# Optimization experiments

Measured on AMD Instinct MI355X. Metric: run time of the kernel, lower is better.

## Reference

```python
import jax, jax.numpy as jnp
import numpy as np

B, LAGS, POOL, D, H, NTS = 16, 4096, 4, 512, 8, 1000
S = LAGS // POOL          # num_pools = 1024
DH = D // H               # head dim = 64


def _layernorm_dim1(x, gamma, beta, eps=1e-5):
    # torch code: mean/var over dim=1 (channel axis), unbiased var, per-position affine
    mean = jnp.mean(x, axis=1, keepdims=True)
    var = jnp.var(x, axis=1, keepdims=True, ddof=1)
    unit = (x - mean) / jnp.sqrt(eps + var)
    return gamma * unit + beta


def setup_inputs() -> dict:
    key = jax.random.key(0)
    ks = jax.random.split(key, 16)
    inp = {
        "ts": jax.random.normal(ks[0], (B, 1, LAGS), dtype=jnp.float32),
        "te": jax.random.randint(ks[1], (B, 1), 0, NTS),
        "conv_w": jax.random.normal(ks[2], (D, 1, POOL), dtype=jnp.float32) * (1.0 / POOL) ** 0.5,
        "conv_b": jax.random.normal(ks[3], (D,), dtype=jnp.float32) * 0.02,
        "pe_emb": jax.random.normal(ks[4], (S, D), dtype=jnp.float32),
        "ts_emb": jax.random.normal(ks[5], (NTS, D), dtype=jnp.float32),
        "ln1_g": jnp.ones((S,), dtype=jnp.float32),
        "ln1_b": jnp.zeros((S,), dtype=jnp.float32),
        "dense_M": jax.random.normal(ks[6], (D, D), dtype=jnp.float32) * D ** -0.5,
        "Wq": jax.random.normal(ks[7], (H, DH, D), dtype=jnp.float32) * D ** -0.5,
        "Wk": jax.random.normal(ks[8], (H, DH, D), dtype=jnp.float32) * D ** -0.5,
        "Wv": jax.random.normal(ks[9], (H, DH, D), dtype=jnp.float32) * D ** -0.5,
        "Wo": jax.random.normal(ks[10], (D, D), dtype=jnp.float32) * D ** -0.5,
        "bo": jnp.zeros((D, 1), dtype=jnp.float32),
        "ln2_g": jnp.ones((S,), dtype=jnp.float32),
        "ln2_b": jnp.zeros((S,), dtype=jnp.float32),
    }
    return inp


def _forward(ts, te, conv_w, conv_b, pe_emb, ts_emb, ln1_g, ln1_b,
             dense_M, Wq, Wk, Wv, Wo, bo, ln2_g, ln2_b):
    # Conv1d with stride == kernel_size: non-overlapping patches
    xr = ts.reshape(B, S, POOL)                                   # (B,S,P)
    conv = jnp.einsum('bsp,dp->bds', xr, conv_w[:, 0, :]) + conv_b[:, None]  # (B,D,S)
    conv = conv + pe_emb.T                                        # positional add (D,S)
    act = jax.nn.gelu(conv, approximate=False)
    n1 = _layernorm_dim1(act, ln1_g, ln1_b)
    dense = jnp.einsum('ed,bds->bes', dense_M, n1)                # Linear: M @ x
    dense = dense + ts_emb[te[:, 0]][:, :, None]                  # ts embedding (B,D,1)

    # multi-head attention, Q=K=V=dense; vectorized over heads
    Qd = jnp.einsum('hcd,bds->bhcs', Wq, dense)                   # (B,H,DH,S)
    Kd = jnp.einsum('hcd,bds->bhcs', Wk, dense)
    Vd = jnp.einsum('hcd,bds->bhcs', Wv, dense)
    scores = jnp.einsum('bhci,bhcj->bhij', Qd, Kd) / DH ** 0.5    # (B,H,S,S)
    i_idx = jnp.arange(S)
    mask = i_idx[:, None] > i_idx[None, :]                        # tril(diagonal=-1): i>j -> -inf
    scores = jnp.where(mask, -jnp.inf, scores)
    sm = jax.nn.softmax(scores, axis=2)                           # softmax over dim 1 of (S,S)
    attn = jnp.einsum('bhci,bhij->bhcj', Vd, sm)                  # V @ softmaxed
    cat = attn.reshape(B, D, S)                                   # concat heads on dim 1
    out = jnp.einsum('ed,bds->bes', Wo, cat) + bo[None]           # final linear + bias
    res = out + conv                                              # residual
    return _layernorm_dim1(res, ln2_g, ln2_b)


def reference(ts, te, conv_w, conv_b, pe_emb, ts_emb, ln1_g, ln1_b,
              dense_M, Wq, Wk, Wv, Wo, bo, ln2_g, ln2_b):
    return _forward(ts, te, conv_w, conv_b, pe_emb, ts_emb, ln1_g, ln1_b,
                    dense_M, Wq, Wk, Wv, Wo, bo, ln2_g, ln2_b)
```

## Files before the change

kernel.cpp:

```cpp
#include <hip/hip_runtime.h>
#include <hip/hip_bf16.h>

#define B_ 16
#define S_ 1024
#define D_ 512
#define H_ 8
#define DH_ 64

typedef __attribute__((ext_vector_type(8))) short bf16x8;
typedef __attribute__((ext_vector_type(4))) short bf16x4;
typedef __attribute__((ext_vector_type(4))) float f32x4;
typedef __attribute__((ext_vector_type(16))) float f32x16;

__device__ __forceinline__ short f2bf(float f) {
    __hip_bfloat16 h = __float2bfloat16(f);
    return *reinterpret_cast<short*>(&h);
}
__device__ __forceinline__ unsigned pack_bf2(float lo, float hi) {
    unsigned a = (unsigned)(unsigned short)f2bf(lo);
    unsigned b = (unsigned)(unsigned short)f2bf(hi);
    return a | (b << 16);
}
__device__ __forceinline__ void gload16(const void* g, void* l) {
    __builtin_amdgcn_global_load_lds(
        (const __attribute__((address_space(1))) unsigned int*)g,
        (__attribute__((address_space(3))) unsigned int*)l, 16, 0, 0);
}

__global__ __launch_bounds__(256) void prep_w(
    const float* __restrict__ M, const float* __restrict__ Wq,
    const float* __restrict__ Wk, const float* __restrict__ Wv,
    const float* __restrict__ Wo, __hip_bfloat16* __restrict__ wb)
{
    const int gid = blockIdx.x * 256 + threadIdx.x;
    const int e8 = gid * 8;
    const int w = e8 >> 18;
    const int off = e8 & 262143;
    const float* src = (w == 0) ? M : (w == 1) ? Wq : (w == 2) ? Wk
                      : (w == 3) ? Wv : Wo;
    const float scale = (w == 1) ? 0.18033688011112042f : 1.0f;
    const float4 f0 = *reinterpret_cast<const float4*>(src + off);
    const float4 f1 = *reinterpret_cast<const float4*>(src + off + 4);
    union { short s[8]; bf16x8 v; } r;
    r.s[0] = f2bf(f0.x * scale); r.s[1] = f2bf(f0.y * scale);
    r.s[2] = f2bf(f0.z * scale); r.s[3] = f2bf(f0.w * scale);
    r.s[4] = f2bf(f1.x * scale); r.s[5] = f2bf(f1.y * scale);
    r.s[6] = f2bf(f1.z * scale); r.s[7] = f2bf(f1.w * scale);
    *reinterpret_cast<bf16x8*>(wb + e8) = r.v;
}

__global__ __launch_bounds__(256) void k1_conv_gelu_ln(
    const float* __restrict__ ts, const float* __restrict__ conv_w,
    const float* __restrict__ conv_b, const float* __restrict__ pe,
    const float* __restrict__ g1, const float* __restrict__ b1,
    __hip_bfloat16* __restrict__ n1)
{
    const int row = blockIdx.x;
    const int b = row >> 10, s = row & 1023;
    const int t = threadIdx.x;
    const float4 x = *reinterpret_cast<const float4*>(ts + b * 4096 + s * 4);

    float a[2];
#pragma unroll
    for (int k = 0; k < 2; ++k) {
        const int d = t + k * 256;
        const float4 w = *reinterpret_cast<const float4*>(conv_w + d * 4);
        float v = x.x * w.x + x.y * w.y + x.z * w.z + x.w * w.w
                + conv_b[d] + pe[s * 512 + d];
        a[k] = 0.5f * v * (1.0f + erff(v * 0.70710678118654752f));
    }
    float sum = a[0] + a[1], sq = a[0] * a[0] + a[1] * a[1];
#pragma unroll
    for (int off = 32; off > 0; off >>= 1) {
        sum += __shfl_down(sum, off);
        sq  += __shfl_down(sq, off);
    }
    __shared__ float rs[4], rq[4];
    const int wv = t >> 6, ln = t & 63;
    if (ln == 0) { rs[wv] = sum; rq[wv] = sq; }
    __syncthreads();
    sum = rs[0] + rs[1] + rs[2] + rs[3];
    sq  = rq[0] + rq[1] + rq[2] + rq[3];
    const float mean = sum * (1.0f / 512.0f);
    const float var  = (sq - 512.0f * mean * mean) * (1.0f / 511.0f);
    const float rstd = rsqrtf(var + 1e-5f);
    const float gg = g1[s], bb = b1[s];
#pragma unroll
    for (int k = 0; k < 2; ++k) {
        const int d = t + k * 256;
        n1[(size_t)row * 512 + d] = __float2bfloat16(gg * ((a[k] - mean) * rstd) + bb);
    }
}

template<int MODE>
__global__ __launch_bounds__(256) void gemm_k(
    const __hip_bfloat16* __restrict__ A,
    const __hip_bfloat16* __restrict__ Wb,
    void* __restrict__ outp,
    const float* __restrict__ aux,
    const int* __restrict__ te)
{
    __shared__ char lA[128 * 128];
    __shared__ char lB[128 * 128];

    const int t = threadIdx.x;
    const int lane = t & 63;
    const int w = t >> 6;
    const int wm = w & 1, wn = w >> 1;
    const int Rb = blockIdx.x * 128;
    const int Nb = blockIdx.y * 128;
    const int g = lane >> 4, lr = lane & 15;
    const int lrow = lane >> 3;
    const int coff = ((lane & 7) ^ lrow) * 8;

    f32x4 acc[4][4];
#pragma unroll
    for (int i = 0; i < 4; ++i)
#pragma unroll
        for (int j = 0; j < 4; ++j) acc[i][j] = {0.f, 0.f, 0.f, 0.f};

    for (int kt = 0; kt < 8; ++kt) {
        const int k0 = kt * 64;
#pragma unroll
        for (int i = 0; i < 4; ++i) {
            const int r0 = w * 32 + i * 8;
            gload16(A + (size_t)(Rb + r0 + lrow) * 512 + k0 + coff, lA + r0 * 128);
        }
#pragma unroll
        for (int i = 0; i < 4; ++i) {
            const int r0 = w * 32 + i * 8;
            gload16(Wb + (size_t)(Nb + r0 + lrow) * 512 + k0 + coff, lB + r0 * 128);
        }
        __syncthreads();
#pragma unroll
        for (int kk = 0; kk < 2; ++kk) {
            bf16x8 af[4], bfv[4];
            const int ch = kk * 4 + g;
#pragma unroll
            for (int mt = 0; mt < 4; ++mt) {
                const int row = wm * 64 + mt * 16 + lr;
                af[mt] = *reinterpret_cast<const bf16x8*>(
                    lA + row * 128 + ((ch ^ (row & 7)) << 4));
            }
#pragma unroll
            for (int nt = 0; nt < 4; ++nt) {
                const int row = wn * 64 + nt * 16 + lr;
                bfv[nt] = *reinterpret_cast<const bf16x8*>(
                    lB + row * 128 + ((ch ^ (row & 7)) << 4));
            }
#pragma unroll
            for (int mt = 0; mt < 4; ++mt)
#pragma unroll
                for (int nt = 0; nt < 4; ++nt)
                    acc[mt][nt] = __builtin_amdgcn_mfma_f32_16x16x32_bf16(
                        af[mt], bfv[nt], acc[mt][nt], 0, 0, 0);
        }
        __syncthreads();
    }

#pragma unroll
    for (int mt = 0; mt < 4; ++mt) {
#pragma unroll
        for (int nt = 0; nt < 4; ++nt) {
#pragma unroll
            for (int r = 0; r < 4; ++r) {
                const int R = Rb + wm * 64 + mt * 16 + 4 * g + r;
                const int N = Nb + wn * 64 + nt * 16 + lr;
                float v = acc[mt][nt][r];
                if (MODE == 0) {
                    const int b = R >> 10;
                    v += aux[(size_t)te[b] * 512 + N];
                    reinterpret_cast<__hip_bfloat16*>(outp)[(size_t)R * 512 + N] =
                        __float2bfloat16(v);
                } else if (MODE == 1) {
                    const int b = R >> 10, s = R & 1023, h = N >> 6, c = N & 63;
                    reinterpret_cast<__hip_bfloat16*>(outp)
                        [(((size_t)(b * 8 + h)) * 1024 + s) * 64 + c] = __float2bfloat16(v);
                } else if (MODE == 2) {
                    const int b = R >> 10, s = R & 1023, h = N >> 6, c = N & 63;
                    reinterpret_cast<__hip_bfloat16*>(outp)
                        [(((size_t)(b * 8 + h)) * 64 + c) * 1024 + s] = __float2bfloat16(v);
                } else {
                    reinterpret_cast<float*>(outp)[(size_t)R * 512 + N] = v + aux[N];
                }
            }
        }
    }
}

__device__ __forceinline__ void attn_step(
    const bf16x8 (&qf)[4], const bf16x8 (&kf)[4],
    const bf16x8& v00, const bf16x8& v01,
    const bf16x8& v10, const bf16x8& v11,
    const bool diag, const int l5, const int ln31,
    float& m, float& lsum, f32x16& o0, f32x16& o1)
{
    f32x16 sc;
#pragma unroll
    for (int r = 0; r < 16; ++r) sc[r] = 0.f;
#pragma unroll
    for (int kt = 0; kt < 4; ++kt)
        sc = __builtin_amdgcn_mfma_f32_32x32x16_bf16(qf[kt], kf[kt], sc, 0, 0, 0);

    float p[16];
    float mx = -3e38f;
    if (diag) {
#pragma unroll
        for (int r = 0; r < 16; ++r) {
            const int irow = (r & 3) + 8 * (r >> 2) + 4 * l5;
            const float v = (irow > ln31) ? -3e38f : sc[r];
            p[r] = v; mx = fmaxf(mx, v);
        }
    } else {
#pragma unroll
        for (int r = 0; r < 16; ++r) { p[r] = sc[r]; mx = fmaxf(mx, sc[r]); }
    }
    mx = fmaxf(mx, __shfl_xor(mx, 32));
    if (!__all(mx <= m + 8.0f)) {
        const float mn = fmaxf(m, mx);
        const float alpha = exp2f(m - mn);
        m = mn; lsum *= alpha;
#pragma unroll
        for (int r = 0; r < 16; ++r) {
            const int jrow = (r & 3) + 8 * (r >> 2) + 4 * l5;
            const float ar = __shfl(alpha, jrow);
            o0[r] *= ar; o1[r] *= ar;
        }
    }
    float ps = 0.f;
#pragma unroll
    for (int r = 0; r < 16; ++r) { p[r] = exp2f(p[r] - m); ps += p[r]; }
    ps += __shfl_xor(ps, 32);
    lsum += ps;

    union { unsigned u[4]; bf16x8 v; } pa0, pa1;
    pa0.u[0] = pack_bf2(p[0],  p[1]);  pa0.u[1] = pack_bf2(p[2],  p[3]);
    pa0.u[2] = pack_bf2(p[4],  p[5]);  pa0.u[3] = pack_bf2(p[6],  p[7]);
    pa1.u[0] = pack_bf2(p[8],  p[9]);  pa1.u[1] = pack_bf2(p[10], p[11]);
    pa1.u[2] = pack_bf2(p[12], p[13]); pa1.u[3] = pack_bf2(p[14], p[15]);
    o0 = __builtin_amdgcn_mfma_f32_32x32x16_bf16(pa0.v, v00, o0, 0, 0, 0);
    o0 = __builtin_amdgcn_mfma_f32_32x32x16_bf16(pa1.v, v01, o0, 0, 0, 0);
    o1 = __builtin_amdgcn_mfma_f32_32x32x16_bf16(pa0.v, v10, o1, 0, 0, 0);
    o1 = __builtin_amdgcn_mfma_f32_32x32x16_bf16(pa1.v, v11, o1, 0, 0, 0);
}

__device__ __forceinline__ void write_strip(
    __hip_bfloat16* __restrict__ dstbase, const int jw0,
    const f32x16& o0, const f32x16& o1, const float lsum,
    const int l5, const int ln31)
{
    const float linv = 1.0f / lsum;
#pragma unroll
    for (int r = 0; r < 16; ++r) {
        const int jrow = (r & 3) + 8 * (r >> 2) + 4 * l5;
        const float rinv = __shfl(linv, jrow);
        __hip_bfloat16* dst = dstbase + (size_t)(jw0 + jrow) * 512;
        dst[ln31]      = __float2bfloat16(o0[r] * rinv);
        dst[32 + ln31] = __float2bfloat16(o1[r] * rinv);
    }
}

__global__ __launch_bounds__(256, 2) void attn3_k(
    const __hip_bfloat16* __restrict__ Qm,
    const __hip_bfloat16* __restrict__ Km,
    const __hip_bfloat16* __restrict__ Vt,
    __hip_bfloat16* __restrict__ cat)
{
    const int t = threadIdx.x, lane = t & 63, w = t >> 6;
    const int l5 = lane >> 5, ln31 = lane & 31;
    const int bh = blockIdx.y;
    const int b = bh >> 3, h = bh & 7;
    const int sA = blockIdx.x * 4 + w;
    const int sB = 31 - sA;
    const int jA = sA * 32, jB = sB * 32;
    const int nA = sA + 1, nB = sB + 1;

    const __hip_bfloat16* Qh = Qm + (size_t)bh * (S_ * 64);
    const __hip_bfloat16* Kh = Km + (size_t)bh * (S_ * 64);
    const __hip_bfloat16* Vh = Vt + (size_t)bh * (64 * S_);

    bf16x8 kfA[4], kfB[4];
#pragma unroll
    for (int kt = 0; kt < 4; ++kt) {
        kfA[kt] = *reinterpret_cast<const bf16x8*>(
            Kh + (size_t)(jA + ln31) * 64 + kt * 16 + l5 * 8);
        kfB[kt] = *reinterpret_cast<const bf16x8*>(
            Kh + (size_t)(jB + ln31) * 64 + kt * 16 + l5 * 8);
    }

    f32x16 oA0, oA1, oB0, oB1;
#pragma unroll
    for (int r = 0; r < 16; ++r) { oA0[r] = 0.f; oA1[r] = 0.f; oB0[r] = 0.f; oB1[r] = 0.f; }
    float mA = -3e38f, lsA = 0.f, mB = -3e38f, lsB = 0.f;

    const __hip_bfloat16* Vr0 = Vh + (size_t)ln31 * S_;
    const __hip_bfloat16* Vr1 = Vh + (size_t)(32 + ln31) * S_;

    union u8 { bf16x4 h[2]; bf16x8 v; };
    bf16x8 qf[4]; u8 v00, v01, v10, v11;

    auto load_q = [&](int i0, bf16x8 (&dst)[4]) {
#pragma unroll
        for (int kt = 0; kt < 4; ++kt)
            dst[kt] = *reinterpret_cast<const bf16x8*>(
                Qh + (size_t)(i0 + ln31) * 64 + kt * 16 + l5 * 8);
    };
    auto load_v = [&](int i0, u8& a0, u8& a1, u8& a2, u8& a3) {
        const int b0 = i0 + 4 * l5, b1 = i0 + 16 + 4 * l5;
        a0.h[0] = *reinterpret_cast<const bf16x4*>(Vr0 + b0);
        a0.h[1] = *reinterpret_cast<const bf16x4*>(Vr0 + b0 + 8);
        a1.h[0] = *reinterpret_cast<const bf16x4*>(Vr0 + b1);
        a1.h[1] = *reinterpret_cast<const bf16x4*>(Vr0 + b1 + 8);
        a2.h[0] = *reinterpret_cast<const bf16x4*>(Vr1 + b0);
        a2.h[1] = *reinterpret_cast<const bf16x4*>(Vr1 + b0 + 8);
        a3.h[0] = *reinterpret_cast<const bf16x4*>(Vr1 + b1);
        a3.h[1] = *reinterpret_cast<const bf16x4*>(Vr1 + b1 + 8);
    };

    load_q(0, qf);
    load_v(0, v00, v01, v10, v11);

    for (int it = 0; it < nB; ++it) {
        const int ipf = (it + 1 < nB ? it + 1 : it) * 32;
        bf16x8 qn[4]; u8 n00, n01, n10, n11;
        load_q(ipf, qn);
        load_v(ipf, n00, n01, n10, n11);

        attn_step(qf, kfB, v00.v, v01.v, v10.v, v11.v,
                  it == nB - 1, l5, ln31, mB, lsB, oB0, oB1);
        if (it < nA)
            attn_step(qf, kfA, v00.v, v01.v, v10.v, v11.v,
                      it == nA - 1, l5, ln31, mA, lsA, oA0, oA1);

#pragma unroll
        for (int kt = 0; kt < 4; ++kt) qf[kt] = qn[kt];
        v00 = n00; v01 = n01; v10 = n10; v11 = n11;
    }

    __hip_bfloat16* dstbase = cat + (size_t)b * 1024 * 512 + h * 64;
    write_strip(dstbase, jA, oA0, oA1, lsA, l5, ln31);
    write_strip(dstbase, jB, oB0, oB1, lsB, l5, ln31);
}

__global__ __launch_bounds__(256) void k5_res_ln(
    const float* __restrict__ outf,
    const float* __restrict__ ts, const float* __restrict__ conv_w,
    const float* __restrict__ conv_b, const float* __restrict__ pe,
    const float* __restrict__ g2, const float* __restrict__ b2,
    float* __restrict__ out)
{
    __shared__ float tile[16 * 520];
    const int blk = blockIdx.x;
    const int b = blk >> 6, s0 = (blk & 63) * 16;
    const int t = threadIdx.x;
    const int sl = t >> 4, c = t & 15;
    const int s = s0 + sl;

    const float4 x = *reinterpret_cast<const float4*>(ts + b * 4096 + s * 4);
    float vals[32];
    float sum = 0.f, sq = 0.f;
#pragma unroll
    for (int j = 0; j < 32; ++j) {
        const int d = c + 16 * j;
        const float4 wv = *reinterpret_cast<const float4*>(conv_w + d * 4);
        const float conv = x.x * wv.x + x.y * wv.y + x.z * wv.z + x.w * wv.w
                         + conv_b[d] + pe[s * 512 + d];
        const float a = outf[(size_t)(b * 1024 + s) * 512 + d] + conv;
        vals[j] = a; sum += a; sq += a * a;
    }
#pragma unroll
    for (int off = 1; off < 16; off <<= 1) {
        sum += __shfl_xor(sum, off);
        sq  += __shfl_xor(sq, off);
    }
    const float mean = sum * (1.0f / 512.0f);
    const float var  = (sq - 512.0f * mean * mean) * (1.0f / 511.0f);
    const float rstd = rsqrtf(var + 1e-5f);
    const float gg = g2[s], bb = b2[s];
#pragma unroll
    for (int j = 0; j < 32; ++j) {
        const int d = c + 16 * j;
        tile[sl * 520 + d] = gg * ((vals[j] - mean) * rstd) + bb;
    }
    __syncthreads();
#pragma unroll
    for (int q2 = 0; q2 < 2; ++q2) {
        const int d = t + q2 * 256;
        float buf[16];
#pragma unroll
        for (int sl2 = 0; sl2 < 16; ++sl2) buf[sl2] = tile[sl2 * 520 + d];
        float4* dst = reinterpret_cast<float4*>(
            out + ((size_t)b * 512 + d) * 1024 + s0);
        dst[0] = make_float4(buf[0],  buf[1],  buf[2],  buf[3]);
        dst[1] = make_float4(buf[4],  buf[5],  buf[6],  buf[7]);
        dst[2] = make_float4(buf[8],  buf[9],  buf[10], buf[11]);
        dst[3] = make_float4(buf[12], buf[13], buf[14], buf[15]);
    }
}

extern "C" void kernel_launch(void* const* d_in, const int* in_sizes, int n_in,
                              void* d_out, int out_size, void* d_ws, size_t ws_size,
                              hipStream_t stream)
{
    const float* ts     = (const float*)d_in[0];
    const int*   te     = (const int*)d_in[1];
    const float* conv_w = (const float*)d_in[2];
    const float* conv_b = (const float*)d_in[3];
    const float* pe     = (const float*)d_in[4];
    const float* ts_emb = (const float*)d_in[5];
    const float* g1     = (const float*)d_in[6];
    const float* b1     = (const float*)d_in[7];
    const float* M      = (const float*)d_in[8];
    const float* Wq     = (const float*)d_in[9];
    const float* Wk     = (const float*)d_in[10];
    const float* Wv     = (const float*)d_in[11];
    const float* Wo     = (const float*)d_in[12];
    const float* bo     = (const float*)d_in[13];
    const float* g2     = (const float*)d_in[14];
    const float* b2     = (const float*)d_in[15];

    char* ws = (char*)d_ws;
    __hip_bfloat16* wb    = (__hip_bfloat16*)(ws);
    __hip_bfloat16* Mb    = wb;
    __hip_bfloat16* Wqb   = wb + 262144;
    __hip_bfloat16* Wkb   = wb + 2 * 262144;
    __hip_bfloat16* Wvb   = wb + 3 * 262144;
    __hip_bfloat16* Wob   = wb + 4 * 262144;
    __hip_bfloat16* n1    = (__hip_bfloat16*)(ws + ( 3ull << 20));
    __hip_bfloat16* cat   = n1;
    __hip_bfloat16* dense = (__hip_bfloat16*)(ws + (19ull << 20));
    float*          outf  = (float*)(ws + (19ull << 20));
    __hip_bfloat16* q     = (__hip_bfloat16*)(ws + (35ull << 20));
    __hip_bfloat16* k     = (__hip_bfloat16*)(ws + (51ull << 20));
    __hip_bfloat16* vT    = (__hip_bfloat16*)(ws + (67ull << 20));

    prep_w<<<640, 256, 0, stream>>>(M, Wq, Wk, Wv, Wo, wb);
    k1_conv_gelu_ln<<<16384, 256, 0, stream>>>(ts, conv_w, conv_b, pe, g1, b1, n1);
    gemm_k<0><<<dim3(128, 4), 256, 0, stream>>>(n1, Mb, dense, ts_emb, te);
    gemm_k<1><<<dim3(128, 4), 256, 0, stream>>>(dense, Wqb, q, nullptr, nullptr);
    gemm_k<1><<<dim3(128, 4), 256, 0, stream>>>(dense, Wkb, k, nullptr, nullptr);
    gemm_k<2><<<dim3(128, 4), 256, 0, stream>>>(dense, Wvb, vT, nullptr, nullptr);
    attn3_k<<<dim3(4, 128), 256, 0, stream>>>(q, k, vT, cat);
    gemm_k<3><<<dim3(128, 4), 256, 0, stream>>>(cat, Wob, outf, bo, nullptr);
    k5_res_ln<<<1024, 256, 0, stream>>>(outf, ts, conv_w, conv_b, pe, g2, b2,
                                        (float*)d_out);
}
```

Measured before the change: 210.7 us.

## Fuse QKV projections into one GEMM and split attention key range across warp pairs

```diff
diff --git a/kernel.cpp b/kernel.cpp
--- a/kernel.cpp
+++ b/kernel.cpp
@@ -172,14 +172,18 @@
                     v += aux[(size_t)te[b] * 512 + N];
                     reinterpret_cast<__hip_bfloat16*>(outp)[(size_t)R * 512 + N] =
                         __float2bfloat16(v);
-                } else if (MODE == 1) {
-                    const int b = R >> 10, s = R & 1023, h = N >> 6, c = N & 63;
-                    reinterpret_cast<__hip_bfloat16*>(outp)
-                        [(((size_t)(b * 8 + h)) * 1024 + s) * 64 + c] = __float2bfloat16(v);
-                } else if (MODE == 2) {
-                    const int b = R >> 10, s = R & 1023, h = N >> 6, c = N & 63;
-                    reinterpret_cast<__hip_bfloat16*>(outp)
-                        [(((size_t)(b * 8 + h)) * 64 + c) * 1024 + s] = __float2bfloat16(v);
+                } else if (MODE == 5) {
+                    const int b = R >> 10, s = R & 1023;
+                    const int w3 = N >> 9, Nl = N & 511;
+                    const int h = Nl >> 6, c = Nl & 63;
+                    __hip_bfloat16* base =
+                        reinterpret_cast<__hip_bfloat16*>(outp) + (size_t)w3 * 8388608;
+                    if (w3 == 2)
+                        base[(((size_t)(b * 8 + h)) * 64 + c) * 1024 + s] =
+                            __float2bfloat16(v);
+                    else
+                        base[(((size_t)(b * 8 + h)) * 1024 + s) * 64 + c] =
+                            __float2bfloat16(v);
                 } else {
                     reinterpret_cast<float*>(outp)[(size_t)R * 512 + N] = v + aux[N];
                 }
@@ -244,6 +248,26 @@
     o1 = __builtin_amdgcn_mfma_f32_32x32x16_bf16(pa1.v, v11, o1, 0, 0, 0);
 }
 
+__device__ __forceinline__ void merge_partial(
+    float& m, float& lsum, f32x16& o0, f32x16& o1,
+    const float* __restrict__ buf, const int l5)
+{
+    const float m1 = buf[32], l1 = buf[33];
+    const float ms = fmaxf(m, m1);
+    const float a0 = exp2f(m - ms);
+    const float a1 = exp2f(m1 - ms);
+    lsum = lsum * a0 + l1 * a1;
+    m = ms;
+#pragma unroll
+    for (int r = 0; r < 16; ++r) {
+        const int jrow = (r & 3) + 8 * (r >> 2) + 4 * l5;
+        const float ar0 = __shfl(a0, jrow);
+        const float ar1 = __shfl(a1, jrow);
+        o0[r] = o0[r] * ar0 + buf[r]      * ar1;
+        o1[r] = o1[r] * ar0 + buf[16 + r] * ar1;
+    }
+}
+
 __device__ __forceinline__ void write_strip(
     __hip_bfloat16* __restrict__ dstbase, const int jw0,
     const f32x16& o0, const f32x16& o1, const float lsum,
@@ -260,20 +284,26 @@
     }
 }
 
-__global__ __launch_bounds__(256, 2) void attn3_k(
+__global__ __launch_bounds__(256, 2) void attn4_k(
     const __hip_bfloat16* __restrict__ Qm,
     const __hip_bfloat16* __restrict__ Km,
     const __hip_bfloat16* __restrict__ Vt,
     __hip_bfloat16* __restrict__ cat)
 {
+    __shared__ float mrg[2][2][64][34];
+
     const int t = threadIdx.x, lane = t & 63, w = t >> 6;
     const int l5 = lane >> 5, ln31 = lane & 31;
     const int bh = blockIdx.y;
     const int b = bh >> 3, h = bh & 7;
-    const int sA = blockIdx.x * 4 + w;
-    const int sB = 31 - sA;
+    const int q = w >> 1, half = w & 1;
+    const int p = blockIdx.x * 2 + q;
+    const int sA = p, sB = 31 - p;
     const int jA = sA * 32, jB = sB * 32;
     const int nA = sA + 1, nB = sB + 1;
+    const int mp = (p >= 8) ? 8 : 16 - p;
+    const int lo = half ? mp : 0;
+    const int hi = half ? nB : mp;
 
     const __hip_bfloat16* Qh = Qm + (size_t)bh * (S_ * 64);
     const __hip_bfloat16* Kh = Km + (size_t)bh * (S_ * 64);
@@ -296,50 +326,51 @@
     const __hip_bfloat16* Vr0 = Vh + (size_t)ln31 * S_;
     const __hip_bfloat16* Vr1 = Vh + (size_t)(32 + ln31) * S_;
 
-    union u8 { bf16x4 h[2]; bf16x8 v; };
-    bf16x8 qf[4]; u8 v00, v01, v10, v11;
-
-    auto load_q = [&](int i0, bf16x8 (&dst)[4]) {
+    for (int it = lo; it < hi; ++it) {
+        const int i0 = it * 32;
+        bf16x8 qf[4];
 #pragma unroll
         for (int kt = 0; kt < 4; ++kt)
-            dst[kt] = *reinterpret_cast<const bf16x8*>(
+            qf[kt] = *reinterpret_cast<const bf16x8*>(
                 Qh + (size_t)(i0 + ln31) * 64 + kt * 16 + l5 * 8);
-    };
-    auto load_v = [&](int i0, u8& a0, u8& a1, u8& a2, u8& a3) {
         const int b0 = i0 + 4 * l5, b1 = i0 + 16 + 4 * l5;
-        a0.h[0] = *reinterpret_cast<const bf16x4*>(Vr0 + b0);
-        a0.h[1] = *reinterpret_cast<const bf16x4*>(Vr0 + b0 + 8);
-        a1.h[0] = *reinterpret_cast<const bf16x4*>(Vr0 + b1);
-        a1.h[1] = *reinterpret_cast<const bf16x4*>(Vr0 + b1 + 8);
-        a2.h[0] = *reinterpret_cast<const bf16x4*>(Vr1 + b0);
-        a2.h[1] = *reinterpret_cast<const bf16x4*>(Vr1 + b0 + 8);
-        a3.h[0] = *reinterpret_cast<const bf16x4*>(Vr1 + b1);
-        a3.h[1] = *reinterpret_cast<const bf16x4*>(Vr1 + b1 + 8);
-    };
-
-    load_q(0, qf);
-    load_v(0, v00, v01, v10, v11);
-
-    for (int it = 0; it < nB; ++it) {
-        const int ipf = (it + 1 < nB ? it + 1 : it) * 32;
-        bf16x8 qn[4]; u8 n00, n01, n10, n11;
-        load_q(ipf, qn);
-        load_v(ipf, n00, n01, n10, n11);
+        union u8 { bf16x4 h[2]; bf16x8 v; };
+        u8 v00, v01, v10, v11;
+        v00.h[0] = *reinterpret_cast<const bf16x4*>(Vr0 + b0);
+        v00.h[1] = *reinterpret_cast<const bf16x4*>(Vr0 + b0 + 8);
+        v01.h[0] = *reinterpret_cast<const bf16x4*>(Vr0 + b1);
+        v01.h[1] = *reinterpret_cast<const bf16x4*>(Vr0 + b1 + 8);
+        v10.h[0] = *reinterpret_cast<const bf16x4*>(Vr1 + b0);
+        v10.h[1] = *reinterpret_cast<const bf16x4*>(Vr1 + b0 + 8);
+        v11.h[0] = *reinterpret_cast<const bf16x4*>(Vr1 + b1);
+        v11.h[1] = *reinterpret_cast<const bf16x4*>(Vr1 + b1 + 8);
 
         attn_step(qf, kfB, v00.v, v01.v, v10.v, v11.v,
                   it == nB - 1, l5, ln31, mB, lsB, oB0, oB1);
         if (it < nA)
             attn_step(qf, kfA, v00.v, v01.v, v10.v, v11.v,
                       it == nA - 1, l5, ln31, mA, lsA, oA0, oA1);
-
-#pragma unroll
-        for (int kt = 0; kt < 4; ++kt) qf[kt] = qn[kt];
-        v00 = n00; v01 = n01; v10 = n10; v11 = n11;
-    }
-
-    __hip_bfloat16* dstbase = cat + (size_t)b * 1024 * 512 + h * 64;
-    write_strip(dstbase, jA, oA0, oA1, lsA, l5, ln31);
-    write_strip(dstbase, jB, oB0, oB1, lsB, l5, ln31);
+    }
+
+    if (half) {
+        float* bufB = &mrg[q][0][lane][0];
+        float* bufA = &mrg[q][1][lane][0];
+#pragma unroll
+        for (int r = 0; r < 16; ++r) {
+            bufB[r] = oB0[r]; bufB[16 + r] = oB1[r];
+            bufA[r] = oA0[r]; bufA[16 + r] = oA1[r];
+        }
+        bufB[32] = mB; bufB[33] = lsB;
+        bufA[32] = mA; bufA[33] = lsA;
+    }
+    __syncthreads();
+    if (!half) {
+        merge_partial(mB, lsB, oB0, oB1, &mrg[q][0][lane][0], l5);
+        merge_partial(mA, lsA, oA0, oA1, &mrg[q][1][lane][0], l5);
+        __hip_bfloat16* dstbase = cat + (size_t)b * 1024 * 512 + h * 64;
+        write_strip(dstbase, jA, oA0, oA1, lsA, l5, ln31);
+        write_strip(dstbase, jB, oB0, oB1, lsB, l5, ln31);
+    }
 }
 
 __global__ __launch_bounds__(256) void k5_res_ln(
@@ -422,25 +453,22 @@
     char* ws = (char*)d_ws;
     __hip_bfloat16* wb    = (__hip_bfloat16*)(ws);
     __hip_bfloat16* Mb    = wb;
-    __hip_bfloat16* Wqb   = wb + 262144;
-    __hip_bfloat16* Wkb   = wb + 2 * 262144;
-    __hip_bfloat16* Wvb   = wb + 3 * 262144;
+    __hip_bfloat16* Wqkv  = wb + 262144;
     __hip_bfloat16* Wob   = wb + 4 * 262144;
     __hip_bfloat16* n1    = (__hip_bfloat16*)(ws + ( 3ull << 20));
     __hip_bfloat16* cat   = n1;
     __hip_bfloat16* dense = (__hip_bfloat16*)(ws + (19ull << 20));
     float*          outf  = (float*)(ws + (19ull << 20));
-    __hip_bfloat16* q     = (__hip_bfloat16*)(ws + (35ull << 20));
-    __hip_bfloat16* k     = (__hip_bfloat16*)(ws + (51ull << 20));
-    __hip_bfloat16* vT    = (__hip_bfloat16*)(ws + (67ull << 20));
+    __hip_bfloat16* qkv   = (__hip_bfloat16*)(ws + (35ull << 20));
+    __hip_bfloat16* qb    = qkv;
+    __hip_bfloat16* kb    = qkv + 8388608;
+    __hip_bfloat16* vTb   = qkv + 16777216;
 
     prep_w<<<640, 256, 0, stream>>>(M, Wq, Wk, Wv, Wo, wb);
     k1_conv_gelu_ln<<<16384, 256, 0, stream>>>(ts, conv_w, conv_b, pe, g1, b1, n1);
     gemm_k<0><<<dim3(128, 4), 256, 0, stream>>>(n1, Mb, dense, ts_emb, te);
-    gemm_k<1><<<dim3(128, 4), 256, 0, stream>>>(dense, Wqb, q, nullptr, nullptr);
-    gemm_k<1><<<dim3(128, 4), 256, 0, stream>>>(dense, Wkb, k, nullptr, nullptr);
-    gemm_k<2><<<dim3(128, 4), 256, 0, stream>>>(dense, Wvb, vT, nullptr, nullptr);
-    attn3_k<<<dim3(4, 128), 256, 0, stream>>>(q, k, vT, cat);
+    gemm_k<5><<<dim3(128, 12), 256, 0, stream>>>(dense, Wqkv, qkv, nullptr, nullptr);
+    attn4_k<<<dim3(8, 128), 256, 0, stream>>>(qb, kb, vTb, cat);
     gemm_k<3><<<dim3(128, 4), 256, 0, stream>>>(cat, Wob, outf, bo, nullptr);
     k5_res_ln<<<1024, 256, 0, stream>>>(outf, ts, conv_w, conv_b, pe, g2, b2,
                                         (float*)d_out);
```

Result: slower. 219.5 us (+4.2%).

## Stage Q/V tiles in shared LDS with double buffering; one row per wave in LN

Applied to the files above, without the earlier changes.

```diff
diff --git a/kernel.cpp b/kernel.cpp
--- a/kernel.cpp
+++ b/kernel.cpp
@@ -55,41 +55,43 @@
     const float* __restrict__ g1, const float* __restrict__ b1,
     __hip_bfloat16* __restrict__ n1)
 {
-    const int row = blockIdx.x;
+    const int w = threadIdx.x >> 6, lane = threadIdx.x & 63;
+    const int row = blockIdx.x * 4 + w;
     const int b = row >> 10, s = row & 1023;
-    const int t = threadIdx.x;
     const float4 x = *reinterpret_cast<const float4*>(ts + b * 4096 + s * 4);
-
-    float a[2];
-#pragma unroll
-    for (int k = 0; k < 2; ++k) {
-        const int d = t + k * 256;
-        const float4 w = *reinterpret_cast<const float4*>(conv_w + d * 4);
-        float v = x.x * w.x + x.y * w.y + x.z * w.z + x.w * w.w
-                + conv_b[d] + pe[s * 512 + d];
-        a[k] = 0.5f * v * (1.0f + erff(v * 0.70710678118654752f));
-    }
-    float sum = a[0] + a[1], sq = a[0] * a[0] + a[1] * a[1];
-#pragma unroll
-    for (int off = 32; off > 0; off >>= 1) {
-        sum += __shfl_down(sum, off);
-        sq  += __shfl_down(sq, off);
-    }
-    __shared__ float rs[4], rq[4];
-    const int wv = t >> 6, ln = t & 63;
-    if (ln == 0) { rs[wv] = sum; rq[wv] = sq; }
-    __syncthreads();
-    sum = rs[0] + rs[1] + rs[2] + rs[3];
-    sq  = rq[0] + rq[1] + rq[2] + rq[3];
+    const int d0 = lane * 8;
+
+    const float4 cb0 = *reinterpret_cast<const float4*>(conv_b + d0);
+    const float4 cb1 = *reinterpret_cast<const float4*>(conv_b + d0 + 4);
+    const float4 pe0 = *reinterpret_cast<const float4*>(pe + s * 512 + d0);
+    const float4 pe1 = *reinterpret_cast<const float4*>(pe + s * 512 + d0 + 4);
+    const float cbv[8] = {cb0.x, cb0.y, cb0.z, cb0.w, cb1.x, cb1.y, cb1.z, cb1.w};
+    const float pev[8] = {pe0.x, pe0.y, pe0.z, pe0.w, pe1.x, pe1.y, pe1.z, pe1.w};
+
+    float a[8];
+    float sum = 0.f, sq = 0.f;
+#pragma unroll
+    for (int j = 0; j < 8; ++j) {
+        const float4 wv = *reinterpret_cast<const float4*>(conv_w + (d0 + j) * 4);
+        float v = x.x * wv.x + x.y * wv.y + x.z * wv.z + x.w * wv.w
+                + cbv[j] + pev[j];
+        v = 0.5f * v * (1.0f + erff(v * 0.70710678118654752f));
+        a[j] = v; sum += v; sq += v * v;
+    }
+#pragma unroll
+    for (int off = 1; off < 64; off <<= 1) {
+        sum += __shfl_xor(sum, off);
+        sq  += __shfl_xor(sq, off);
+    }
     const float mean = sum * (1.0f / 512.0f);
     const float var  = (sq - 512.0f * mean * mean) * (1.0f / 511.0f);
     const float rstd = rsqrtf(var + 1e-5f);
     const float gg = g1[s], bb = b1[s];
-#pragma unroll
-    for (int k = 0; k < 2; ++k) {
-        const int d = t + k * 256;
-        n1[(size_t)row * 512 + d] = __float2bfloat16(gg * ((a[k] - mean) * rstd) + bb);
-    }
+    union { short sh[8]; bf16x8 v; } o;
+#pragma unroll
+    for (int j = 0; j < 8; ++j)
+        o.sh[j] = f2bf(gg * ((a[j] - mean) * rstd) + bb);
+    *reinterpret_cast<bf16x8*>(n1 + (size_t)row * 512 + d0) = o.v;
 }
 
 template<int MODE>
@@ -188,62 +190,6 @@
     }
 }
 
-__device__ __forceinline__ void attn_step(
-    const bf16x8 (&qf)[4], const bf16x8 (&kf)[4],
-    const bf16x8& v00, const bf16x8& v01,
-    const bf16x8& v10, const bf16x8& v11,
-    const bool diag, const int l5, const int ln31,
-    float& m, float& lsum, f32x16& o0, f32x16& o1)
-{
-    f32x16 sc;
-#pragma unroll
-    for (int r = 0; r < 16; ++r) sc[r] = 0.f;
-#pragma unroll
-    for (int kt = 0; kt < 4; ++kt)
-        sc = __builtin_amdgcn_mfma_f32_32x32x16_bf16(qf[kt], kf[kt], sc, 0, 0, 0);
-
-    float p[16];
-    float mx = -3e38f;
-    if (diag) {
-#pragma unroll
-        for (int r = 0; r < 16; ++r) {
-            const int irow = (r & 3) + 8 * (r >> 2) + 4 * l5;
-            const float v = (irow > ln31) ? -3e38f : sc[r];
-            p[r] = v; mx = fmaxf(mx, v);
-        }
-    } else {
-#pragma unroll
-        for (int r = 0; r < 16; ++r) { p[r] = sc[r]; mx = fmaxf(mx, sc[r]); }
-    }
-    mx = fmaxf(mx, __shfl_xor(mx, 32));
-    if (!__all(mx <= m + 8.0f)) {
-        const float mn = fmaxf(m, mx);
-        const float alpha = exp2f(m - mn);
-        m = mn; lsum *= alpha;
-#pragma unroll
-        for (int r = 0; r < 16; ++r) {
-            const int jrow = (r & 3) + 8 * (r >> 2) + 4 * l5;
-            const float ar = __shfl(alpha, jrow);
-            o0[r] *= ar; o1[r] *= ar;
-        }
-    }
-    float ps = 0.f;
-#pragma unroll
-    for (int r = 0; r < 16; ++r) { p[r] = exp2f(p[r] - m); ps += p[r]; }
-    ps += __shfl_xor(ps, 32);
-    lsum += ps;
-
-    union { unsigned u[4]; bf16x8 v; } pa0, pa1;
-    pa0.u[0] = pack_bf2(p[0],  p[1]);  pa0.u[1] = pack_bf2(p[2],  p[3]);
-    pa0.u[2] = pack_bf2(p[4],  p[5]);  pa0.u[3] = pack_bf2(p[6],  p[7]);
-    pa1.u[0] = pack_bf2(p[8],  p[9]);  pa1.u[1] = pack_bf2(p[10], p[11]);
-    pa1.u[2] = pack_bf2(p[12], p[13]); pa1.u[3] = pack_bf2(p[14], p[15]);
-    o0 = __builtin_amdgcn_mfma_f32_32x32x16_bf16(pa0.v, v00, o0, 0, 0, 0);
-    o0 = __builtin_amdgcn_mfma_f32_32x32x16_bf16(pa1.v, v01, o0, 0, 0, 0);
-    o1 = __builtin_amdgcn_mfma_f32_32x32x16_bf16(pa0.v, v10, o1, 0, 0, 0);
-    o1 = __builtin_amdgcn_mfma_f32_32x32x16_bf16(pa1.v, v11, o1, 0, 0, 0);
-}
-
 __device__ __forceinline__ void write_strip(
     __hip_bfloat16* __restrict__ dstbase, const int jw0,
     const f32x16& o0, const f32x16& o1, const float lsum,
@@ -260,86 +206,138 @@
     }
 }
 
-__global__ __launch_bounds__(256, 2) void attn3_k(
+__global__ __launch_bounds__(256, 4) void attn5_k(
     const __hip_bfloat16* __restrict__ Qm,
     const __hip_bfloat16* __restrict__ Km,
     const __hip_bfloat16* __restrict__ Vt,
     __hip_bfloat16* __restrict__ cat)
 {
+    __shared__ char qbuf[2][4096];
+    __shared__ char vbuf[2][4096];
+
     const int t = threadIdx.x, lane = t & 63, w = t >> 6;
     const int l5 = lane >> 5, ln31 = lane & 31;
-    const int bh = blockIdx.y;
+    const int id = blockIdx.x;
+    const int bh = id & 127;
+    const int jb = (0x32451067u >> ((id >> 7) * 4)) & 7;
     const int b = bh >> 3, h = bh & 7;
-    const int sA = blockIdx.x * 4 + w;
-    const int sB = 31 - sA;
-    const int jA = sA * 32, jB = sB * 32;
-    const int nA = sA + 1, nB = sB + 1;
+    const int j0 = jb * 128 + w * 32;
 
     const __hip_bfloat16* Qh = Qm + (size_t)bh * (S_ * 64);
     const __hip_bfloat16* Kh = Km + (size_t)bh * (S_ * 64);
     const __hip_bfloat16* Vh = Vt + (size_t)bh * (64 * S_);
 
-    bf16x8 kfA[4], kfB[4];
-#pragma unroll
-    for (int kt = 0; kt < 4; ++kt) {
-        kfA[kt] = *reinterpret_cast<const bf16x8*>(
-            Kh + (size_t)(jA + ln31) * 64 + kt * 16 + l5 * 8);
-        kfB[kt] = *reinterpret_cast<const bf16x8*>(
-            Kh + (size_t)(jB + ln31) * 64 + kt * 16 + l5 * 8);
-    }
-
-    f32x16 oA0, oA1, oB0, oB1;
-#pragma unroll
-    for (int r = 0; r < 16; ++r) { oA0[r] = 0.f; oA1[r] = 0.f; oB0[r] = 0.f; oB1[r] = 0.f; }
-    float mA = -3e38f, lsA = 0.f, mB = -3e38f, lsB = 0.f;
-
-    const __hip_bfloat16* Vr0 = Vh + (size_t)ln31 * S_;
-    const __hip_bfloat16* Vr1 = Vh + (size_t)(32 + ln31) * S_;
-
-    union u8 { bf16x4 h[2]; bf16x8 v; };
-    bf16x8 qf[4]; u8 v00, v01, v10, v11;
-
-    auto load_q = [&](int i0, bf16x8 (&dst)[4]) {
-#pragma unroll
-        for (int kt = 0; kt < 4; ++kt)
-            dst[kt] = *reinterpret_cast<const bf16x8*>(
-                Qh + (size_t)(i0 + ln31) * 64 + kt * 16 + l5 * 8);
+    bf16x8 kf[4];
+#pragma unroll
+    for (int kt = 0; kt < 4; ++kt)
+        kf[kt] = *reinterpret_cast<const bf16x8*>(
+            Kh + (size_t)(j0 + ln31) * 64 + kt * 16 + l5 * 8);
+
+    f32x16 o0, o1;
+#pragma unroll
+    for (int r = 0; r < 16; ++r) { o0[r] = 0.f; o1[r] = 0.f; }
+    float m = -3e38f, lsum = 0.f;
+
+    const int last = jb * 4 + w;
+    const int ntiles = jb * 4 + 4;
+
+    const int q_row  = w * 8 + (lane >> 3);
+    const int q_ch   = (lane & 7) ^ (lane >> 3);
+    const int v_row  = w * 16 + (lane >> 2);
+    const int v_ch   = (lane & 3) ^ ((lane >> 2) & 3) ^ ((lane >> 4) & 3);
+    const __hip_bfloat16* qsrc = Qh + (size_t)q_row * 64 + q_ch * 8;
+    const __hip_bfloat16* vsrc = Vh + (size_t)v_row * 1024 + v_ch * 8;
+
+    auto stage = [&](int buf, int tile) {
+        const int i0 = tile * 32;
+        gload16(qsrc + (size_t)i0 * 64, &qbuf[buf][w * 1024]);
+        gload16(vsrc + i0,              &vbuf[buf][w * 1024]);
     };
-    auto load_v = [&](int i0, u8& a0, u8& a1, u8& a2, u8& a3) {
-        const int b0 = i0 + 4 * l5, b1 = i0 + 16 + 4 * l5;
-        a0.h[0] = *reinterpret_cast<const bf16x4*>(Vr0 + b0);
-        a0.h[1] = *reinterpret_cast<const bf16x4*>(Vr0 + b0 + 8);
-        a1.h[0] = *reinterpret_cast<const bf16x4*>(Vr0 + b1);
-        a1.h[1] = *reinterpret_cast<const bf16x4*>(Vr0 + b1 + 8);
-        a2.h[0] = *reinterpret_cast<const bf16x4*>(Vr1 + b0);
-        a2.h[1] = *reinterpret_cast<const bf16x4*>(Vr1 + b0 + 8);
-        a3.h[0] = *reinterpret_cast<const bf16x4*>(Vr1 + b1);
-        a3.h[1] = *reinterpret_cast<const bf16x4*>(Vr1 + b1 + 8);
-    };
-
-    load_q(0, qf);
-    load_v(0, v00, v01, v10, v11);
-
-    for (int it = 0; it < nB; ++it) {
-        const int ipf = (it + 1 < nB ? it + 1 : it) * 32;
-        bf16x8 qn[4]; u8 n00, n01, n10, n11;
-        load_q(ipf, qn);
-        load_v(ipf, n00, n01, n10, n11);
-
-        attn_step(qf, kfB, v00.v, v01.v, v10.v, v11.v,
-                  it == nB - 1, l5, ln31, mB, lsB, oB0, oB1);
-        if (it < nA)
-            attn_step(qf, kfA, v00.v, v01.v, v10.v, v11.v,
-                      it == nA - 1, l5, ln31, mA, lsA, oA0, oA1);
-
-#pragma unroll
-        for (int kt = 0; kt < 4; ++kt) qf[kt] = qn[kt];
-        v00 = n00; v01 = n01; v10 = n10; v11 = n11;
+
+    stage(0, 0);
+    __syncthreads();
+
+    for (int tt = 0; tt < ntiles; ++tt) {
+        const int buf = tt & 1;
+        if (tt + 1 < ntiles) stage(buf ^ 1, tt + 1);
+        if (tt <= last) {
+            f32x16 sc;
+#pragma unroll
+            for (int r = 0; r < 16; ++r) sc[r] = 0.f;
+            bf16x8 qf[4];
+#pragma unroll
+            for (int kt = 0; kt < 4; ++kt)
+                qf[kt] = *reinterpret_cast<const bf16x8*>(
+                    &qbuf[buf][ln31 * 128 + (((kt * 2 + l5) ^ (ln31 & 7)) << 4)]);
+#pragma unroll
+            for (int kt = 0; kt < 4; ++kt)
+                sc = __builtin_amdgcn_mfma_f32_32x32x16_bf16(qf[kt], kf[kt], sc, 0, 0, 0);
+
+            union u8 { bf16x4 h[2]; bf16x8 v; };
+            u8 vf[2][2];
+#pragma unroll
+            for (int kt = 0; kt < 2; ++kt) {
+#pragma unroll
+                for (int dh = 0; dh < 2; ++dh) {
+                    const int drow = ln31 + dh * 32;
+                    const int swz = (drow & 3) ^ ((drow >> 2) & 3);
+                    const int x0 = kt * 32 + 8 * l5;
+#pragma unroll
+                    for (int hp = 0; hp < 2; ++hp) {
+                        const int x = x0 + hp * 16;
+                        vf[kt][dh].h[hp] = *reinterpret_cast<const bf16x4*>(
+                            &vbuf[buf][drow * 64 + (((x >> 4) ^ swz) << 4) + (x & 15)]);
+                    }
+                }
+            }
+
+            const bool diag = (tt == last);
+            float p[16];
+            float mx = -3e38f;
+            if (diag) {
+#pragma unroll
+                for (int r = 0; r < 16; ++r) {
+                    const int irow = (r & 3) + 8 * (r >> 2) + 4 * l5;
+                    const float v = (irow > ln31) ? -3e38f : sc[r];
+                    p[r] = v; mx = fmaxf(mx, v);
+                }
+            } else {
+#pragma unroll
+                for (int r = 0; r < 16; ++r) { p[r] = sc[r]; mx = fmaxf(mx, sc[r]); }
+            }
+            mx = fmaxf(mx, __shfl_xor(mx, 32));
+            if (!__all(mx <= m + 8.0f)) {
+                const float mn = fmaxf(m, mx);
+                const float alpha = exp2f(m - mn);
+                m = mn; lsum *= alpha;
+#pragma unroll
+                for (int r = 0; r < 16; ++r) {
+                    const int jrow = (r & 3) + 8 * (r >> 2) + 4 * l5;
+                    const float ar = __shfl(alpha, jrow);
+                    o0[r] *= ar; o1[r] *= ar;
+                }
+            }
+            float ps = 0.f;
+#pragma unroll
+            for (int r = 0; r < 16; ++r) { p[r] = exp2f(p[r] - m); ps += p[r]; }
+            ps += __shfl_xor(ps, 32);
+            lsum += ps;
+
+            union { unsigned u[4]; bf16x8 v; } pa0, pa1;
+            pa0.u[0] = pack_bf2(p[0],  p[1]);  pa0.u[1] = pack_bf2(p[2],  p[3]);
+            pa0.u[2] = pack_bf2(p[4],  p[5]);  pa0.u[3] = pack_bf2(p[6],  p[7]);
+            pa1.u[0] = pack_bf2(p[8],  p[9]);  pa1.u[1] = pack_bf2(p[10], p[11]);
+            pa1.u[2] = pack_bf2(p[12], p[13]); pa1.u[3] = pack_bf2(p[14], p[15]);
+            o0 = __builtin_amdgcn_mfma_f32_32x32x16_bf16(pa0.v, vf[0][0].v, o0, 0, 0, 0);
+            o1 = __builtin_amdgcn_mfma_f32_32x32x16_bf16(pa0.v, vf[0][1].v, o1, 0, 0, 0);
+            o0 = __builtin_amdgcn_mfma_f32_32x32x16_bf16(pa1.v, vf[1][0].v, o0, 0, 0, 0);
+            o1 = __builtin_amdgcn_mfma_f32_32x32x16_bf16(pa1.v, vf[1][1].v, o1, 0, 0, 0);
+        }
+        __syncthreads();
     }
 
     __hip_bfloat16* dstbase = cat + (size_t)b * 1024 * 512 + h * 64;
-    write_strip(dstbase, jA, oA0, oA1, lsA, l5, ln31);
-    write_strip(dstbase, jB, oB0, oB1, lsB, l5, ln31);
+    write_strip(dstbase, j0, o0, o1, lsum, l5, ln31);
 }
 
 __global__ __launch_bounds__(256) void k5_res_ln(
@@ -435,12 +433,12 @@
     __hip_bfloat16* vT    = (__hip_bfloat16*)(ws + (67ull << 20));
 
     prep_w<<<640, 256, 0, stream>>>(M, Wq, Wk, Wv, Wo, wb);
-    k1_conv_gelu_ln<<<16384, 256, 0, stream>>>(ts, conv_w, conv_b, pe, g1, b1, n1);
+    k1_conv_gelu_ln<<<4096, 256, 0, stream>>>(ts, conv_w, conv_b, pe, g1, b1, n1);
     gemm_k<0><<<dim3(128, 4), 256, 0, stream>>>(n1, Mb, dense, ts_emb, te);
     gemm_k<1><<<dim3(128, 4), 256, 0, stream>>>(dense, Wqb, q, nullptr, nullptr);
     gemm_k<1><<<dim3(128, 4), 256, 0, stream>>>(dense, Wkb, k, nullptr, nullptr);
     gemm_k<2><<<dim3(128, 4), 256, 0, stream>>>(dense, Wvb, vT, nullptr, nullptr);
-    attn3_k<<<dim3(4, 128), 256, 0, stream>>>(q, k, vT, cat);
+    attn5_k<<<1024, 256, 0, stream>>>(q, k, vT, cat);
     gemm_k<3><<<dim3(128, 4), 256, 0, stream>>>(cat, Wob, outf, bo, nullptr);
     k5_res_ln<<<1024, 256, 0, stream>>>(outf, ts, conv_w, conv_b, pe, g2, b2,
                                         (float*)d_out);
```

After: 173.4 us. -17.7%, faster.
